# Performance work log

Measured on AMD Instinct MI355X. Metric: run time of the kernel, lower is better.

## Reference

```python
import jax, jax.numpy as jnp
import numpy as np

B, S, D = 1, 2048, 1024
F = 1408            # expert intermediate dim
E = 16              # num experts
K = 2               # top_k
CAP_FACTOR = 1.25


def _mlp(h, wg, wu, wd):
    # DeepSeek-style gated MLP (SwiGLU, no bias)
    return (jax.nn.silu(h @ wg) * (h @ wu)) @ wd


def setup_inputs() -> dict:
    key = jax.random.key(0)
    ks = jax.random.split(key, 10)
    sd = 0.02
    return {
        "x": jax.random.normal(ks[0], (B, S, D), jnp.float32),
        "router_w": jax.random.normal(ks[1], (D, E), jnp.float32) * sd,
        "router_b": jnp.zeros((E,), jnp.float32),
        "w_gate": jax.random.normal(ks[2], (E, D, F), jnp.float32) * sd,
        "w_up": jax.random.normal(ks[3], (E, D, F), jnp.float32) * sd,
        "w_down": jax.random.normal(ks[4], (E, F, D), jnp.float32) * sd,
        "sw_gate": jax.random.normal(ks[5], (D, F), jnp.float32) * sd,
        "sw_up": jax.random.normal(ks[6], (D, F), jnp.float32) * sd,
        "sw_down": jax.random.normal(ks[7], (F, D), jnp.float32) * sd,
    }


def reference(x, router_w, router_b, w_gate, w_up, w_down, sw_gate, sw_up, sw_down):
    b, s, d = x.shape
    N = b * s
    NK = N * K
    C = int(np.ceil(CAP_FACTOR * NK / E))  # per-expert capacity

    x_tokens = x.reshape(N, d)

    # Router: softmax -> top-k -> renormalize
    logits = x_tokens @ router_w + router_b           # [N, E]
    probs = jax.nn.softmax(logits, axis=-1)
    vals, idx = jax.lax.top_k(probs, K)               # [N, K]
    vals = vals / (jnp.sum(vals, axis=-1, keepdims=True) + 1e-9)
    idx_flat = idx.reshape(NK)                        # int expert ids
    vals_flat = vals.reshape(NK)

    # Position within each expert's buffer = rank in flattened (token, k) order.
    # Same math as (cumsum(one_hot)*one_hot).sum(-1)-1 in the original.
    oh_e = jax.nn.one_hot(idx_flat, E, dtype=x.dtype)             # [NK, E] (small)
    pos = (jnp.cumsum(oh_e, axis=0) * oh_e).sum(axis=1) - 1       # [NK]
    within = (pos < C).astype(x.dtype)                            # capacity mask
    pos_c = jnp.clip(pos, 0, C - 1).astype(jnp.int32)

    # Dispatch: scatter tokens into per-expert buffers. Positions are unique
    # per expert, so scatter-add equals the dense one-hot einsum exactly.
    token_ids = jnp.arange(NK) // K
    x_pair = x_tokens[token_ids] * within[:, None]                # [NK, D]
    expert_inputs = jnp.zeros((E, C, d), x.dtype).at[idx_flat, pos_c].add(x_pair)

    # Grouped expert MLPs
    expert_outputs = jax.vmap(_mlp)(expert_inputs, w_gate, w_up, w_down)  # [E, C, D]

    # Combine: gather back and weight by renormalized router probs
    gathered = expert_outputs[idx_flat, pos_c] * (vals_flat * within)[:, None]
    output_tokens = gathered.reshape(N, K, d).sum(axis=1)         # [N, D]

    return x + _mlp(x, sw_gate, sw_up, sw_down) + output_tokens.reshape(b, s, d)
```

## Files before the change

### kernel.cpp

```cpp
#include <hip/hip_runtime.h>
#include <hip/hip_bf16.h>

#define TOKENS 2048
#define DIM    1024
#define FDIM   1408
#define NEXP   16
#define NK     (TOKENS * 2)
#define CAP    320
#define RPAD   384

typedef __attribute__((ext_vector_type(4))) float f32x4;
typedef __attribute__((ext_vector_type(2))) float f32x2;
typedef __attribute__((ext_vector_type(8))) short s16x8;
typedef __attribute__((ext_vector_type(4))) short s16x4;

__device__ __forceinline__ short f2bf(float f) {
    unsigned int u = __float_as_uint(f);
    u += 0x7FFFu + ((u >> 16) & 1u);
    return (short)(u >> 16);
}
__device__ __forceinline__ float bf2f(short s) {
    return __uint_as_float(((unsigned int)(unsigned short)s) << 16);
}

#define GLDS16(gp, lp) __builtin_amdgcn_global_load_lds(                     \
    (const __attribute__((address_space(1))) unsigned int*)(gp),             \
    (__attribute__((address_space(3))) unsigned int*)(lp), 16, 0, 0)

struct GSeg {
    const short* A; long aStride; int aRpad;
    const float* B0; const float* B1; long bStride;
    short* Out; long oStride; int oRpad;
    const int* cnt; int Mb, Nb, N, K, nblocks;
};

__global__ __launch_bounds__(256) void router_kernel(
    const float* __restrict__ x, const float* __restrict__ rw,
    const float* __restrict__ rb, int* __restrict__ idx_flat,
    float* __restrict__ vals_flat)
{
    __shared__ float lg[16][17];
    const int t  = threadIdx.x;
    const int tl = t >> 4;
    const int e  = t & 15;
    const int token = blockIdx.x * 16 + tl;
    const float* xr = x + (size_t)token * DIM;

    float acc = 0.f;
    for (int d4 = 0; d4 < DIM / 4; d4++) {
        float4 xv = *(const float4*)(xr + d4 * 4);
        acc += xv.x * rw[(d4 * 4 + 0) * NEXP + e];
        acc += xv.y * rw[(d4 * 4 + 1) * NEXP + e];
        acc += xv.z * rw[(d4 * 4 + 2) * NEXP + e];
        acc += xv.w * rw[(d4 * 4 + 3) * NEXP + e];
    }
    lg[tl][e] = acc + rb[e];
    __syncthreads();

    if (t < 16) {
        float l[16];
#pragma unroll
        for (int j = 0; j < 16; j++) l[j] = lg[t][j];
        float m = l[0];
#pragma unroll
        for (int j = 1; j < 16; j++) m = fmaxf(m, l[j]);
        float p[16], den = 0.f;
#pragma unroll
        for (int j = 0; j < 16; j++) { p[j] = __expf(l[j] - m); den += p[j]; }
        int i1 = -1; float b1 = -1e30f;
#pragma unroll
        for (int j = 0; j < 16; j++) if (p[j] > b1) { b1 = p[j]; i1 = j; }
        int i2 = -1; float b2 = -1e30f;
#pragma unroll
        for (int j = 0; j < 16; j++) if (j != i1 && p[j] > b2) { b2 = p[j]; i2 = j; }
        float v1 = b1 / den, v2 = b2 / den;
        float s = v1 + v2 + 1e-9f;
        int tok = blockIdx.x * 16 + t;
        idx_flat[tok * 2 + 0] = i1;
        idx_flat[tok * 2 + 1] = i2;
        vals_flat[tok * 2 + 0] = v1 / s;
        vals_flat[tok * 2 + 1] = v2 / s;
    }
}

__global__ void scan_kernel(const int* __restrict__ idx_flat,
                            const float* __restrict__ vals,
                            int* __restrict__ dst, float* __restrict__ wgt,
                            int* __restrict__ cnt)
{
    const int lane = threadIdx.x;
    int base[16];
#pragma unroll
    for (int e = 0; e < 16; e++) base[e] = 0;

    for (int c = 0; c < NK / 64; c++) {
        int i = c * 64 + lane;
        int e = idx_flat[i];
        unsigned long long m[16];
#pragma unroll
        for (int ee = 0; ee < 16; ee++) m[ee] = __ballot(e == ee);
        unsigned long long mym = 0ULL; int myb = 0;
#pragma unroll
        for (int ee = 0; ee < 16; ee++) {
            bool sel = (e == ee);
            mym = sel ? m[ee] : mym;
            myb = sel ? base[ee] : myb;
        }
        int pos = myb + (int)__popcll(mym & ((1ULL << lane) - 1ULL));
        bool within = pos < CAP;
        dst[i] = within ? (e * RPAD + pos) : -1;
        wgt[i] = within ? vals[i] : 0.f;
#pragma unroll
        for (int ee = 0; ee < 16; ee++) base[ee] += (int)__popcll(m[ee]);
    }
    if (lane < 16) cnt[lane] = base[lane] < CAP ? base[lane] : CAP;
}

__device__ void xconv_dev(const float* __restrict__ x, short* __restrict__ xb, int bid)
{
    const int token = bid * 2 + (threadIdx.x >> 7);
    const int c = threadIdx.x & 127;
    const float* src = x + (size_t)token * DIM + c * 8;
    float4 v0 = *(const float4*)(src);
    float4 v1 = *(const float4*)(src + 4);
    s16x8 o;
    o[0] = f2bf(v0.x); o[1] = f2bf(v0.y); o[2] = f2bf(v0.z); o[3] = f2bf(v0.w);
    o[4] = f2bf(v1.x); o[5] = f2bf(v1.y); o[6] = f2bf(v1.z); o[7] = f2bf(v1.w);
    *(s16x8*)(xb + (size_t)c * (TOKENS * 8) + (size_t)token * 8) = o;
}

__device__ void scatter_dev(const float* __restrict__ x, const int* __restrict__ dst,
                            const int* __restrict__ idx_flat, short* __restrict__ ex,
                            int bid)
{
    const int i = bid * 2 + (threadIdx.x >> 7);
    const int d0 = dst[i];
    if (d0 < 0) return;
    const int e = idx_flat[i];
    const int pos = d0 - e * RPAD;
    const int token = i >> 1;
    const int c = threadIdx.x & 127;
    const float* src = x + (size_t)token * DIM + c * 8;
    float4 v0 = *(const float4*)(src);
    float4 v1 = *(const float4*)(src + 4);
    s16x8 o;
    o[0] = f2bf(v0.x); o[1] = f2bf(v0.y); o[2] = f2bf(v0.z); o[3] = f2bf(v0.w);
    o[4] = f2bf(v1.x); o[5] = f2bf(v1.y); o[6] = f2bf(v1.z); o[7] = f2bf(v1.w);
    *(s16x8*)(ex + (size_t)e * (DIM * RPAD) + (size_t)c * (RPAD * 8) +
              (size_t)pos * 8) = o;
}

__global__ __launch_bounds__(256) void mid_kernel(
    const float* __restrict__ x, short* __restrict__ xb,
    const int* __restrict__ dst, const int* __restrict__ idx_flat,
    short* __restrict__ ex)
{
    int bid = blockIdx.x;
    if (bid < TOKENS / 2) { xconv_dev(x, xb, bid); return; }
    scatter_dev(x, dst, idx_flat, ex, bid - TOKENS / 2);
}

template <int NMAT>
__device__ void gemm_dev(const GSeg& S, int bid)
{
    constexpr int BUFS = 4096 * (1 + NMAT);
    __shared__ short lds[2 * BUFS];

    const int cpx = S.nblocks >> 3;
    const int lid = (bid & 7) * cpx + (bid >> 3);
    const int mb  = lid % S.Mb;
    const int t1  = lid / S.Mb;
    const int nb  = t1 % S.Nb;
    const int g   = t1 / S.Nb;
    const int m0 = mb * 128, n0 = nb * 128;
    if (S.cnt != nullptr && m0 >= S.cnt[g]) return;

    const int tid = threadIdx.x, lane = tid & 63, w = tid >> 6;
    const int wr = w >> 1, wc = w & 1, ln = lane & 15, kg = lane >> 4;
    const int N = S.N, K = S.K;

    const short* Ag  = S.A  + (size_t)g * S.aStride + (size_t)m0 * 8;
    const float* Bg0 = S.B0 + (size_t)g * S.bStride + n0;
    const float* Bg1 = nullptr;
    if constexpr (NMAT == 2) Bg1 = S.B1 + (size_t)g * S.bStride + n0;

    const size_t aR8 = (size_t)S.aRpad * 8;

    const int srow = tid & 127, sslab = tid >> 7;
    const short* aS0 = Ag + sslab * aR8 + srow * 8;
    const short* aS1 = Ag + (2 + sslab) * aR8 + srow * 8;
    const int dA0 = w * 512, dA1 = 2048 + w * 512;

    const float* bSrc;
    int rB, cW;
    if constexpr (NMAT == 2) {
        const int c4 = tid & 31, gq = (tid >> 5) & 3, mat = tid >> 7;
        bSrc = (mat ? Bg1 : Bg0) + (size_t)gq * 8 * N + c4 * 4;
        rB = 4096 + mat * 4096 + gq * 1024;
        cW = c4;
    } else {
        const int c2 = tid & 63, gq = tid >> 6;
        bSrc = Bg0 + (size_t)gq * 8 * N + c2 * 2;
        rB = 4096 + gq * 1024;
        cW = c2;
    }

    f32x4 bq[8];
    f32x2 bd[8];

    auto LOADB = [&](int ks) {
        const float* p = bSrc + (size_t)ks * 32 * N;
        if constexpr (NMAT == 2) {
#pragma unroll
            for (int j = 0; j < 8; j++) bq[j] = *(const f32x4*)(p + (size_t)j * N);
        } else {
#pragma unroll
            for (int j = 0; j < 8; j++) bd[j] = *(const f32x2*)(p + (size_t)j * N);
        }
    };
    auto STGA = [&](int buf, int ks) {
        const size_t ka = (size_t)ks * 4 * aR8;
        short* base = lds + buf * BUFS;
        GLDS16(aS0 + ka, base + dA0);
        GLDS16(aS1 + ka, base + dA1);
    };
    auto WRITEB = [&](int buf) {
        short* d = lds + buf * BUFS + rB;
        if constexpr (NMAT == 2) {
#pragma unroll
            for (int j = 0; j < 4; j++) {
                const int colS = (cW * 4 + j) ^ ((cW >> 1) & 7);
                s16x8 o;
#pragma unroll
                for (int i = 0; i < 8; i++) o[i] = f2bf(bq[i][j]);
                *(s16x8*)(d + colS * 8) = o;
            }
        } else {
#pragma unroll
            for (int j = 0; j < 2; j++) {
                const int colS = (cW * 2 + j) ^ ((cW >> 2) & 7);
                s16x8 o;
#pragma unroll
                for (int i = 0; i < 8; i++) o[i] = f2bf(bd[i][j]);
                *(s16x8*)(d + colS * 8) = o;
            }
        }
    };

    const int aO = kg * 1024 + (wr * 64 + ln) * 8;

    f32x4 acc[NMAT][4][4] = {};
    const int nt = K / 32;

    LOADB(0);
    __builtin_amdgcn_sched_barrier(0);
    STGA(0, 0);
    __builtin_amdgcn_sched_barrier(0);
    WRITEB(0);
    asm volatile("s_waitcnt lgkmcnt(0)" ::: "memory");
    __builtin_amdgcn_sched_barrier(0);
    LOADB(1);
    __builtin_amdgcn_sched_barrier(0);
    STGA(1, 1);
    __builtin_amdgcn_sched_barrier(0);

    int cur = 0;
    for (int ks = 0; ks < nt; ks++) {
        if (ks + 1 < nt) asm volatile("s_waitcnt vmcnt(10)" ::: "memory");
        else             asm volatile("s_waitcnt vmcnt(0)"  ::: "memory");
        __builtin_amdgcn_s_barrier();
        __builtin_amdgcn_sched_barrier(0);

        const short* base = lds + cur * BUFS;
        s16x8 af[4];
#pragma unroll
        for (int m = 0; m < 4; m++)
            af[m] = *(const s16x8*)(base + aO + m * 128);
        s16x8 bf[NMAT][4];
#pragma unroll
        for (int nf = 0; nf < 4; nf++) {
            const int col  = wc * 64 + nf * 16 + ln;
            const int colS = col ^ ((col >> 3) & 7);
#pragma unroll
            for (int mat = 0; mat < NMAT; mat++)
                bf[mat][nf] = *(const s16x8*)(base + 4096 + mat * 4096 +
                                              kg * 1024 + colS * 8);
        }

#pragma unroll
        for (int nf = 0; nf < 4; nf++)
#pragma unroll
            for (int m = 0; m < 4; m++)
#pragma unroll
                for (int mat = 0; mat < NMAT; mat++)
                    acc[mat][m][nf] = __builtin_amdgcn_mfma_f32_16x16x32_bf16(
                        af[m], bf[mat][nf], acc[mat][m][nf], 0, 0, 0);

        if (ks + 1 < nt) WRITEB(cur ^ 1);

        __builtin_amdgcn_sched_barrier(0);
        asm volatile("s_waitcnt lgkmcnt(0)" ::: "memory");
        __builtin_amdgcn_s_barrier();

        if (ks + 2 < nt) {
            LOADB(ks + 2);
            __builtin_amdgcn_sched_barrier(0);
            STGA(cur, ks + 2);
            __builtin_amdgcn_sched_barrier(0);
        }
        cur ^= 1;
    }

#pragma unroll
    for (int m = 0; m < 4; m++) {
#pragma unroll
        for (int nf = 0; nf < 4; nf++) {
            const int row = m0 + wr * 64 + m * 16 + kg * 4;
            const int col = n0 + wc * 64 + nf * 16 + ln;
#pragma unroll
            for (int j = 0; j < 4; j++) {
                if constexpr (NMAT == 2) {
                    float gv = acc[0][m][nf][j];
                    float uv = acc[1][m][nf][j];
                    float v = gv / (1.f + __expf(-gv)) * uv;
                    S.Out[(size_t)g * S.oStride + (size_t)(col >> 3) * (S.oRpad * 8) +
                          (size_t)(row + j) * 8 + (col & 7)] = f2bf(v);
                } else {
                    S.Out[(size_t)g * S.oStride + (size_t)(row + j) * N + col] =
                        f2bf(acc[0][m][nf][j]);
                }
            }
        }
    }
}

__global__ __launch_bounds__(256, 2) void gateup_kernel(GSeg s0, GSeg s1)
{
    int bid = blockIdx.x;
    if (bid < s0.nblocks) { gemm_dev<2>(s0, bid); return; }
    gemm_dev<2>(s1, bid - s0.nblocks);
}

__global__ __launch_bounds__(256, 2) void down_kernel(GSeg s0, GSeg s1)
{
    int bid = blockIdx.x;
    if (bid < s0.nblocks) { gemm_dev<1>(s0, bid); return; }
    gemm_dev<1>(s1, bid - s0.nblocks);
}

__global__ __launch_bounds__(256) void combine_kernel(
    const float* __restrict__ x, const short* __restrict__ shout,
    const short* __restrict__ eout, const int* __restrict__ dst,
    const float* __restrict__ wgt, float* __restrict__ out)
{
    const int t = blockIdx.x;
    const int d = threadIdx.x * 4;
    size_t o = (size_t)t * DIM + d;
    float4 xv = *(const float4*)(x + o);
    s16x4 sv = *(const s16x4*)(shout + o);
    float r0 = xv.x + bf2f(sv[0]);
    float r1 = xv.y + bf2f(sv[1]);
    float r2 = xv.z + bf2f(sv[2]);
    float r3 = xv.w + bf2f(sv[3]);
#pragma unroll
    for (int k = 0; k < 2; k++) {
        int di = dst[t * 2 + k];
        if (di >= 0) {
            float wv = wgt[t * 2 + k];
            s16x4 ev = *(const s16x4*)(eout + (size_t)di * DIM + d);
            r0 += wv * bf2f(ev[0]);
            r1 += wv * bf2f(ev[1]);
            r2 += wv * bf2f(ev[2]);
            r3 += wv * bf2f(ev[3]);
        }
    }
    float4 rv = {r0, r1, r2, r3};
    *(float4*)(out + o) = rv;
}

extern "C" void kernel_launch(void* const* d_in, const int* in_sizes, int n_in,
                              void* d_out, int out_size, void* d_ws, size_t ws_size,
                              hipStream_t stream)
{
    const float* x   = (const float*)d_in[0];
    const float* rw  = (const float*)d_in[1];
    const float* rb  = (const float*)d_in[2];
    const float* wg  = (const float*)d_in[3];
    const float* wu  = (const float*)d_in[4];
    const float* wd  = (const float*)d_in[5];
    const float* swg = (const float*)d_in[6];
    const float* swu = (const float*)d_in[7];
    const float* swd = (const float*)d_in[8];
    float* out = (float*)d_out;

    char* wp = (char*)d_ws;
    auto alloc = [&](size_t b) { char* p = wp; wp += (b + 255) & ~(size_t)255; return p; };
    int*   idx_flat = (int*)alloc((size_t)NK * 4);
    float* vals     = (float*)alloc((size_t)NK * 4);
    int*   dst      = (int*)alloc((size_t)NK * 4);
    float* wgt      = (float*)alloc((size_t)NK * 4);
    int*   cnt      = (int*)alloc(64);
    short* xb       = (short*)alloc((size_t)TOKENS * DIM * 2);
    short* ex       = (short*)alloc((size_t)NEXP * RPAD * DIM * 2);
    short* acte     = (short*)alloc((size_t)NEXP * RPAD * FDIM * 2);
    short* acts     = (short*)alloc((size_t)TOKENS * FDIM * 2);
    short* eout     = (short*)alloc((size_t)NEXP * RPAD * DIM * 2);
    short* shout    = (short*)alloc((size_t)TOKENS * DIM * 2);

    router_kernel<<<TOKENS / 16, 256, 0, stream>>>(x, rw, rb, idx_flat, vals);
    scan_kernel<<<1, 64, 0, stream>>>(idx_flat, vals, dst, wgt, cnt);

    mid_kernel<<<TOKENS / 2 + NK / 2, 256, 0, stream>>>(x, xb, dst, idx_flat, ex);

    GSeg segGE = {ex, (long)RPAD * DIM, RPAD, wg, wu, (long)DIM * FDIM,
                  acte, (long)RPAD * FDIM, RPAD, cnt, 3, 11, FDIM, DIM, 3 * 11 * NEXP};
    GSeg segGS = {xb, 0L, TOKENS, swg, swu, 0L,
                  acts, 0L, TOKENS, nullptr, 16, 11, FDIM, DIM, 16 * 11};
    gateup_kernel<<<segGE.nblocks + segGS.nblocks, 256, 0, stream>>>(segGE, segGS);

    GSeg segDE = {acte, (long)RPAD * FDIM, RPAD, wd, nullptr, (long)DIM * FDIM,
                  eout, (long)RPAD * DIM, 0, cnt, 3, 8, DIM, FDIM, 3 * 8 * NEXP};
    GSeg segDS = {acts, 0L, TOKENS, swd, nullptr, 0L,
                  shout, 0L, 0, nullptr, 16, 8, DIM, FDIM, 16 * 8};
    down_kernel<<<segDE.nblocks + segDS.nblocks, 256, 0, stream>>>(segDE, segDS);

    combine_kernel<<<TOKENS, 256, 0, stream>>>(x, shout, eout, dst, wgt, out);
}
```

Baseline: 244.7 us.

## Pre-convert down weights to bf16 in gate-up launch and use 64-row LDS-DMA down GEMM

Adds weight-conversion blocks to the gate/up kernel that turn the fp32 down-projection weights into a k-chunked bf16 layout. The down GEMM is rewritten to stage both A and B directly into LDS with global_load_lds, using 64x128 tiles and higher occupancy. It also packs the bf16 conversion with the hardware pair-convert routine and moves the B global loads earlier in the fused gate/up pipeline. This removes the fp32 loads and register conversion from the down GEMM inner loop. In exchange it adds an extra weight write and read pass, and the gate-up launch has to carry that conversion work.

```diff
diff --git a/kernel.cpp b/kernel.cpp
--- a/kernel.cpp
+++ b/kernel.cpp
@@ -22,17 +22,53 @@
 __device__ __forceinline__ float bf2f(short s) {
     return __uint_as_float(((unsigned int)(unsigned short)s) << 16);
 }
+__device__ __forceinline__ unsigned int f2bf_pk(float lo, float hi) {
+    union { __hip_bfloat162 h; unsigned int u; } c;
+    c.h = __float22bfloat162_rn(make_float2(lo, hi));
+    return c.u;
+}
 
 #define GLDS16(gp, lp) __builtin_amdgcn_global_load_lds(                     \
     (const __attribute__((address_space(1))) unsigned int*)(gp),             \
     (__attribute__((address_space(3))) unsigned int*)(lp), 16, 0, 0)
 
-struct GSeg {
+struct GSegF {
     const short* A; long aStride; int aRpad;
     const float* B0; const float* B1; long bStride;
     short* Out; long oStride; int oRpad;
     const int* cnt; int Mb, Nb, N, K, nblocks;
 };
+struct GSegB {
+    const short* A; long aStride; int aRpad;
+    const short* B0; long bStride;
+    short* Out; long oStride;
+    const int* cnt; int Mb, Nb, N, K, nblocks;
+};
+struct WSeg { const float* in; short* out; int K, N, mats, nblocks; };
+
+__device__ void wchunk_dev(const WSeg& W, int bid)
+{
+    const int spm = W.K >> 3;
+    const int mat = bid / spm, s = bid % spm;
+    const float* in  = W.in  + (size_t)mat * W.K * W.N + (size_t)s * 8 * W.N;
+    short* out = W.out + (size_t)mat * W.K * W.N + (size_t)s * W.N * 8;
+    const int t = threadIdx.x;
+    const int iters = (W.N + 511) >> 9;
+    for (int it = 0; it < iters; it++) {
+        const int n = it * 512 + 2 * t;
+        if (n >= W.N) break;
+        const float* src = in + n;
+        s16x8 o0, o1;
+#pragma unroll
+        for (int j = 0; j < 8; j++) {
+            float2 v = *(const float2*)(src + (size_t)j * W.N);
+            o0[j] = f2bf(v.x);
+            o1[j] = f2bf(v.y);
+        }
+        *(s16x8*)(out + (size_t)n * 8)     = o0;
+        *(s16x8*)(out + (size_t)n * 8 + 8) = o1;
+    }
+}
 
 __global__ __launch_bounds__(256) void router_kernel(
     const float* __restrict__ x, const float* __restrict__ rw,
@@ -161,7 +197,7 @@
 }
 
 template <int NMAT>
-__device__ void gemm_dev(const GSeg& S, int bid)
+__device__ void gemm_fused_dev(const GSegF& S, int bid)
 {
     constexpr int BUFS = 4096 * (1 + NMAT);
     __shared__ short lds[2 * BUFS];
@@ -230,19 +266,23 @@
 #pragma unroll
             for (int j = 0; j < 4; j++) {
                 const int colS = (cW * 4 + j) ^ ((cW >> 1) & 7);
-                s16x8 o;
-#pragma unroll
-                for (int i = 0; i < 8; i++) o[i] = f2bf(bq[i][j]);
-                *(s16x8*)(d + colS * 8) = o;
+                uint4 o;
+                o.x = f2bf_pk(bq[0][j], bq[1][j]);
+                o.y = f2bf_pk(bq[2][j], bq[3][j]);
+                o.z = f2bf_pk(bq[4][j], bq[5][j]);
+                o.w = f2bf_pk(bq[6][j], bq[7][j]);
+                *(uint4*)(d + colS * 8) = o;
             }
         } else {
 #pragma unroll
             for (int j = 0; j < 2; j++) {
                 const int colS = (cW * 2 + j) ^ ((cW >> 2) & 7);
-                s16x8 o;
-#pragma unroll
-                for (int i = 0; i < 8; i++) o[i] = f2bf(bd[i][j]);
-                *(s16x8*)(d + colS * 8) = o;
+                uint4 o;
+                o.x = f2bf_pk(bd[0][j], bd[1][j]);
+                o.y = f2bf_pk(bd[2][j], bd[3][j]);
+                o.z = f2bf_pk(bd[4][j], bd[5][j]);
+                o.w = f2bf_pk(bd[6][j], bd[7][j]);
+                *(uint4*)(d + colS * 8) = o;
             }
         }
     };
@@ -257,10 +297,10 @@
     STGA(0, 0);
     __builtin_amdgcn_sched_barrier(0);
     WRITEB(0);
-    asm volatile("s_waitcnt lgkmcnt(0)" ::: "memory");
     __builtin_amdgcn_sched_barrier(0);
     LOADB(1);
     __builtin_amdgcn_sched_barrier(0);
+    asm volatile("s_waitcnt lgkmcnt(0)" ::: "memory");
     STGA(1, 1);
     __builtin_amdgcn_sched_barrier(0);
 
@@ -299,12 +339,12 @@
         if (ks + 1 < nt) WRITEB(cur ^ 1);
 
         __builtin_amdgcn_sched_barrier(0);
+        if (ks + 2 < nt) LOADB(ks + 2);
+        __builtin_amdgcn_sched_barrier(0);
         asm volatile("s_waitcnt lgkmcnt(0)" ::: "memory");
         __builtin_amdgcn_s_barrier();
 
         if (ks + 2 < nt) {
-            LOADB(ks + 2);
-            __builtin_amdgcn_sched_barrier(0);
             STGA(cur, ks + 2);
             __builtin_amdgcn_sched_barrier(0);
         }
@@ -334,18 +374,113 @@
     }
 }
 
-__global__ __launch_bounds__(256, 2) void gateup_kernel(GSeg s0, GSeg s1)
+__device__ void gemm_glds64_dev(const GSegB& S, int bid)
+{
+    constexpr int BUFS = 6144;
+    __shared__ short lds[2 * BUFS];
+
+    const int cpx = S.nblocks >> 3;
+    const int lid = (bid & 7) * cpx + (bid >> 3);
+    const int mb  = lid % S.Mb;
+    const int t1  = lid / S.Mb;
+    const int nb  = t1 % S.Nb;
+    const int g   = t1 / S.Nb;
+    const int m0 = mb * 64, n0 = nb * 128;
+    if (S.cnt != nullptr && m0 >= S.cnt[g]) return;
+
+    const int tid = threadIdx.x, lane = tid & 63, w = tid >> 6;
+    const int wr = w >> 1, wc = w & 1, ln = lane & 15, kg = lane >> 4;
+    const int N = S.N, K = S.K;
+
+    const short* Ag = S.A  + (size_t)g * S.aStride + (size_t)m0 * 8;
+    const short* Bg = S.B0 + (size_t)g * S.bStride + (size_t)n0 * 8;
+
+    const size_t aR8 = (size_t)S.aRpad * 8;
+    const size_t n8  = (size_t)N * 8;
+
+    const short* aS  = Ag + (size_t)(tid >> 6) * aR8 + (size_t)(tid & 63) * 8;
+    const short* bS0 = Bg + (size_t)(tid >> 7) * n8 + (size_t)(tid & 127) * 8;
+    const short* bS1 = Bg + (size_t)((tid >> 7) + 2) * n8 + (size_t)(tid & 127) * 8;
+
+    const int dA  = w * 512;
+    const int dB0 = 2048 + w * 512;
+    const int dB1 = 4096 + w * 512;
+
+    auto STG = [&](int buf, int ks) {
+        const size_t ka = (size_t)ks * 4 * aR8;
+        const size_t kb = (size_t)ks * 4 * n8;
+        short* base = lds + buf * BUFS;
+        GLDS16(aS + ka,  base + dA);
+        GLDS16(bS0 + kb, base + dB0);
+        GLDS16(bS1 + kb, base + dB1);
+    };
+
+    const int aO = kg * 512 + (wr * 32 + ln) * 8;
+    const int bO = 2048 + kg * 1024 + (wc * 64 + ln) * 8;
+
+    f32x4 acc[2][4] = {};
+    const int nt = K / 32;
+    STG(0, 0); STG(1, 1);
+    int cur = 0;
+    for (int ks = 0; ks < nt; ks++) {
+        if (ks + 1 < nt) asm volatile("s_waitcnt vmcnt(3)" ::: "memory");
+        else             asm volatile("s_waitcnt vmcnt(0)" ::: "memory");
+        __builtin_amdgcn_s_barrier();
+        __builtin_amdgcn_sched_barrier(0);
+
+        const short* base = lds + cur * BUFS;
+        s16x8 af[2];
+        af[0] = *(const s16x8*)(base + aO);
+        af[1] = *(const s16x8*)(base + aO + 128);
+        s16x8 bf[4];
+#pragma unroll
+        for (int nf = 0; nf < 4; nf++)
+            bf[nf] = *(const s16x8*)(base + bO + nf * 128);
+
+#pragma unroll
+        for (int nf = 0; nf < 4; nf++)
+#pragma unroll
+            for (int m = 0; m < 2; m++)
+                acc[m][nf] = __builtin_amdgcn_mfma_f32_16x16x32_bf16(
+                    af[m], bf[nf], acc[m][nf], 0, 0, 0);
+
+        __builtin_amdgcn_sched_barrier(0);
+        __builtin_amdgcn_s_barrier();
+        if (ks + 2 < nt) STG(cur, ks + 2);
+        cur ^= 1;
+    }
+
+#pragma unroll
+    for (int m = 0; m < 2; m++) {
+#pragma unroll
+        for (int nf = 0; nf < 4; nf++) {
+            const int row = m0 + wr * 32 + m * 16 + kg * 4;
+            const int col = n0 + wc * 64 + nf * 16 + ln;
+#pragma unroll
+            for (int j = 0; j < 4; j++)
+                S.Out[(size_t)g * S.oStride + (size_t)(row + j) * N + col] =
+                    f2bf(acc[m][nf][j]);
+        }
+    }
+}
+
+__global__ __launch_bounds__(256, 2) void gateup_kernel(GSegF s0, GSegF s1,
+                                                        WSeg w0, WSeg w1)
 {
     int bid = blockIdx.x;
-    if (bid < s0.nblocks) { gemm_dev<2>(s0, bid); return; }
-    gemm_dev<2>(s1, bid - s0.nblocks);
-}
-
-__global__ __launch_bounds__(256, 2) void down_kernel(GSeg s0, GSeg s1)
+    if (bid < s0.nblocks) { gemm_fused_dev<2>(s0, bid); return; }
+    bid -= s0.nblocks;
+    if (bid < s1.nblocks) { gemm_fused_dev<2>(s1, bid); return; }
+    bid -= s1.nblocks;
+    if (bid < w0.nblocks) { wchunk_dev(w0, bid); return; }
+    wchunk_dev(w1, bid - w0.nblocks);
+}
+
+__global__ __launch_bounds__(256, 4) void down_kernel(GSegB s0, GSegB s1)
 {
     int bid = blockIdx.x;
-    if (bid < s0.nblocks) { gemm_dev<1>(s0, bid); return; }
-    gemm_dev<1>(s1, bid - s0.nblocks);
+    if (bid < s0.nblocks) { gemm_glds64_dev(s0, bid); return; }
+    gemm_glds64_dev(s1, bid - s0.nblocks);
 }
 
 __global__ __launch_bounds__(256) void combine_kernel(
@@ -406,22 +541,27 @@
     short* acts     = (short*)alloc((size_t)TOKENS * FDIM * 2);
     short* eout     = (short*)alloc((size_t)NEXP * RPAD * DIM * 2);
     short* shout    = (short*)alloc((size_t)TOKENS * DIM * 2);
+    short* wdC      = (short*)alloc((size_t)NEXP * DIM * FDIM * 2);
+    short* swdC     = (short*)alloc((size_t)DIM * FDIM * 2);
 
     router_kernel<<<TOKENS / 16, 256, 0, stream>>>(x, rw, rb, idx_flat, vals);
     scan_kernel<<<1, 64, 0, stream>>>(idx_flat, vals, dst, wgt, cnt);
 
     mid_kernel<<<TOKENS / 2 + NK / 2, 256, 0, stream>>>(x, xb, dst, idx_flat, ex);
 
-    GSeg segGE = {ex, (long)RPAD * DIM, RPAD, wg, wu, (long)DIM * FDIM,
-                  acte, (long)RPAD * FDIM, RPAD, cnt, 3, 11, FDIM, DIM, 3 * 11 * NEXP};
-    GSeg segGS = {xb, 0L, TOKENS, swg, swu, 0L,
-                  acts, 0L, TOKENS, nullptr, 16, 11, FDIM, DIM, 16 * 11};
-    gateup_kernel<<<segGE.nblocks + segGS.nblocks, 256, 0, stream>>>(segGE, segGS);
-
-    GSeg segDE = {acte, (long)RPAD * FDIM, RPAD, wd, nullptr, (long)DIM * FDIM,
-                  eout, (long)RPAD * DIM, 0, cnt, 3, 8, DIM, FDIM, 3 * 8 * NEXP};
-    GSeg segDS = {acts, 0L, TOKENS, swd, nullptr, 0L,
-                  shout, 0L, 0, nullptr, 16, 8, DIM, FDIM, 16 * 8};
+    GSegF segGE = {ex, (long)RPAD * DIM, RPAD, wg, wu, (long)DIM * FDIM,
+                   acte, (long)RPAD * FDIM, RPAD, cnt, 3, 11, FDIM, DIM, 3 * 11 * NEXP};
+    GSegF segGS = {xb, 0L, TOKENS, swg, swu, 0L,
+                   acts, 0L, TOKENS, nullptr, 16, 11, FDIM, DIM, 16 * 11};
+    WSeg Wd  = {wd,  wdC,  FDIM, DIM, NEXP, NEXP * (FDIM / 8)};
+    WSeg Wsd = {swd, swdC, FDIM, DIM, 1,    FDIM / 8};
+    gateup_kernel<<<segGE.nblocks + segGS.nblocks + Wd.nblocks + Wsd.nblocks,
+                    256, 0, stream>>>(segGE, segGS, Wd, Wsd);
+
+    GSegB segDE = {acte, (long)RPAD * FDIM, RPAD, wdC, (long)DIM * FDIM,
+                   eout, (long)RPAD * DIM, cnt, 6, 8, DIM, FDIM, 6 * 8 * NEXP};
+    GSegB segDS = {acts, 0L, TOKENS, swdC, 0L,
+                   shout, 0L, nullptr, 32, 8, DIM, FDIM, 32 * 8};
     down_kernel<<<segDE.nblocks + segDS.nblocks, 256, 0, stream>>>(segDE, segDS);
 
     combine_kernel<<<TOKENS, 256, 0, stream>>>(x, shout, eout, dst, wgt, out);
```

Result: faster. 230.7 us (-5.7%).
